# Performance work log

Measured on AMD Instinct MI355X. Metric: run time of the kernel, lower is better.

Reference implementation:

```python
import jax, jax.numpy as jnp
import numpy as np

B, NX, NY = 8, 256, 256
WIDTH, HIDDEN, M1, M2, NLAYERS = 32, 128, 16, 16, 4


def setup_inputs() -> dict:
    key = jax.random.key(0)
    ks = jax.random.split(key, 16)
    scale = 1.0 / (WIDTH * WIDTH)
    inp = {
        'bc': jax.random.normal(ks[0], (B, 3), jnp.float32),
        'x': jax.random.uniform(ks[1], (B, NX, NY), jnp.float32),
        'y': jax.random.uniform(ks[2], (B, NX, NY), jnp.float32),
        'mlp1_w': jax.random.normal(ks[3], (5, WIDTH), jnp.float32) * 0.3,
        'mlp1_b': jnp.zeros((WIDTH,), jnp.float32),
        'spec_wr': scale * jax.random.normal(ks[4], (NLAYERS, WIDTH, WIDTH, M1, M2), jnp.float32),
        'spec_wi': scale * jax.random.normal(ks[5], (NLAYERS, WIDTH, WIDTH, M1, M2), jnp.float32),
        'pw_w': jax.random.normal(ks[6], (NLAYERS, WIDTH, WIDTH), jnp.float32) * (1.0 / np.sqrt(WIDTH)),
        'pw_b': jnp.zeros((NLAYERS, WIDTH), jnp.float32),
        'dec_w1': jax.random.normal(ks[7], (3, WIDTH, WIDTH), jnp.float32) * (1.0 / np.sqrt(WIDTH)),
        'dec_b1': jnp.zeros((3, WIDTH), jnp.float32),
        'dec_w2': jax.random.normal(ks[8], (3, WIDTH, HIDDEN), jnp.float32) * (1.0 / np.sqrt(WIDTH)),
        'dec_b2': jnp.zeros((3, HIDDEN), jnp.float32),
        'dec_w3': jax.random.normal(ks[9], (3, HIDDEN, 1), jnp.float32) * (1.0 / np.sqrt(HIDDEN)),
        'dec_b3': jnp.zeros((3, 1), jnp.float32),
    }
    return inp


def _gelu(v):
    return jax.nn.gelu(v, approximate=False)  # torch F.gelu default = exact erf


def _spectral_conv(h, wr, wi):
    # h: (B, C, NX, NY)
    w = wr + 1j * wi  # (C, C, M1, M2)
    x_ft = jnp.fft.rfft2(h, norm='ortho')  # (B, C, NX, NY//2+1)
    t = jnp.einsum('bixy,ioxy->boxy', x_ft[:, :, :M1, :M2], w)
    out_ft = jnp.zeros((h.shape[0], wr.shape[1], NX, NY // 2 + 1), jnp.complex64)
    out_ft = out_ft.at[:, :, :M1, :M2].set(t)
    return jnp.fft.irfft2(out_ft, s=(NX, NY), norm='ortho')


def reference(bc, x, y, mlp1_w, mlp1_b, spec_wr, spec_wi, pw_w, pw_b,
              dec_w1, dec_b1, dec_w2, dec_b2, dec_w3, dec_b3):
    Bsz, Nx, Ny = x.shape
    bc_exp = jnp.broadcast_to(bc[:, None, None, :], (Bsz, Nx, Ny, 3))
    inp = jnp.concatenate([bc_exp, x[..., None], y[..., None]], axis=-1)  # (B,Nx,Ny,5)
    h = inp @ mlp1_w + mlp1_b  # lifting
    h = jnp.transpose(h, (0, 3, 1, 2))  # (B, W, Nx, Ny)
    for l in range(NLAYERS):
        sc = _spectral_conv(h, spec_wr[l], spec_wi[l])
        pw = jnp.einsum('bixy,oi->boxy', h, pw_w[l]) + pw_b[l][None, :, None, None]
        h = h + _gelu(sc + pw)
    hf = jnp.transpose(h, (0, 2, 3, 1))  # (B, Nx, Ny, W)
    outs = []
    for d in range(3):  # temp, pressure, velocity decoders
        z = _gelu(hf @ dec_w1[d] + dec_b1[d])
        z = _gelu(z @ dec_w2[d] + dec_b2[d])
        outs.append(z @ dec_w3[d] + dec_b3[d])  # (B,Nx,Ny,1)
    return jnp.concatenate(outs, axis=-1)
```

## Files before the change

### kernel.cpp

```cpp
#include <hip/hip_runtime.h>
#include <math.h>

#define BSZ 8
#define CW  32
#define NN  256
#define MM  16
#define NL  4
#define HID 128

typedef __attribute__((ext_vector_type(8))) short bf16x8;
typedef __attribute__((ext_vector_type(4))) short s16x4;
typedef __attribute__((ext_vector_type(4))) float f32x4;
typedef __attribute__((ext_vector_type(4))) unsigned int u32x4;

static __device__ __forceinline__ float gelu_f(float v) {
    float av = fabsf(v);
    float u  = av * 0.70710678118654752f;
    float P  = fmaf(fmaf(fmaf(fmaf(0.078108f, u, 0.000972f), u, 0.230389f),
                         u, 0.278393f), u, 1.0f);
    float r  = __builtin_amdgcn_rcpf(P);
    float r2 = r * r;
    float r4 = r2 * r2;
    return fmaf(-0.5f * av, r4, fmaxf(v, 0.0f));
}

static __device__ __forceinline__ unsigned pack_hl(float v) {
    unsigned b  = __float_as_uint(v);
    unsigned hi = b >> 16;
    float hif   = __uint_as_float(hi << 16);
    float lo    = v - hif;
    unsigned lou = __float_as_uint(lo) >> 16;
    return (hi << 16) | lou;
}

static __device__ __forceinline__ short bf16_rne(float v) {
    unsigned u = __float_as_uint(v);
    u += 0x7fffu + ((u >> 16) & 1u);
    return (short)(u >> 16);
}

#define TWO_PI_OVER_N (6.28318530717958647692f / 256.0f)

__global__ void k_prep(const float* __restrict__ w1, const float* __restrict__ w2,
                       const float* __restrict__ pww,
                       short* __restrict__ wb1h, short* __restrict__ wb1l,
                       short* __restrict__ wb2h, short* __restrict__ wb2l,
                       short* __restrict__ wpwh, short* __restrict__ wpwl,
                       short* __restrict__ wifh, short* __restrict__ wifl,
                       short* __restrict__ wfyh, short* __restrict__ wfyl) {
    int t0 = blockIdx.x * 256 + threadIdx.x;
    for (int idx = t0; idx < 3 * 2 * 16 * 32; idx += 8192) {
        int k = idx & 31, n16 = (idx >> 5) & 15, nb = (idx >> 9) & 1, d = idx >> 10;
        unsigned p = pack_hl(w1[d * 1024 + k * 32 + nb * 16 + n16]);
        wb1h[idx] = (short)(p >> 16);
        wb1l[idx] = (short)(p & 0xffffu);
    }
    for (int idx = t0; idx < 3 * 8 * 16 * 32; idx += 8192) {
        int k = idx & 31, n16 = (idx >> 5) & 15, blk = (idx >> 9) & 7, d = idx >> 12;
        unsigned p = pack_hl(w2[d * 4096 + k * 128 + blk * 16 + n16]);
        wb2h[idx] = (short)(p >> 16);
        wb2l[idx] = (short)(p & 0xffffu);
    }
    for (int idx = t0; idx < NL * 1024; idx += 8192) {
        unsigned p = pack_hl(pww[idx]);
        wpwh[idx] = (short)(p >> 16);
        wpwl[idx] = (short)(p & 0xffffu);
    }
    for (int idx = t0; idx < 16 * 64 * 8; idx += 8192) {
        int j = idx & 7, l = (idx >> 3) & 63, ntg = idx >> 9;
        int k = ((l >> 4) << 3) + j, y = (ntg << 4) + (l & 15);
        int ky = k >> 1, p = k & 1;
        float v;
        if (k == 0)      v = 1.0f / 256.0f;
        else if (k == 1) v = 0.0f;
        else {
            float ang = TWO_PI_OVER_N * (float)((ky * y) & 255);
            v = p ? (-2.0f / 256.0f) * sinf(ang) : (2.0f / 256.0f) * cosf(ang);
        }
        unsigned pb = pack_hl(v);
        wifh[idx] = (short)(pb >> 16);
        wifl[idx] = (short)(pb & 0xffffu);
    }
    for (int idx = t0; idx < 16 * 64 * 8; idx += 8192) {
        int j = idx & 7, l = (idx >> 3) & 63, f = idx >> 9;
        int nt = f & 1, kstep = f >> 1;
        int y  = (kstep >> 1) * 64 + (kstep & 1) * 32 + ((l >> 4) << 3) + j;
        int kc = nt * 16 + (l & 15);
        int ky = kc >> 1, p = kc & 1;
        float ang = TWO_PI_OVER_N * (float)((ky * y) & 255);
        float v = p ? -sinf(ang) : cosf(ang);
        unsigned pb = pack_hl(v);
        wfyh[idx] = (short)(pb >> 16);
        wfyl[idx] = (short)(pb & 0xffffu);
    }
}

static __device__ __forceinline__ void dft_y_mfma(
        const short* __restrict__ hlsh, const short* __restrict__ hlsl,
        float* __restrict__ red,
        const short* __restrict__ wfyh, const short* __restrict__ wfyl,
        float* __restrict__ gy, int b, int x, int wv, int lk, int l15, int tid) {
    f32x4 acc2[2][2];
#pragma unroll
    for (int mt = 0; mt < 2; ++mt)
#pragma unroll
        for (int nt = 0; nt < 2; ++nt) acc2[mt][nt] = (f32x4){0.f, 0.f, 0.f, 0.f};
#pragma unroll
    for (int kk = 0; kk < 2; ++kk) {
        bf16x8 ahh[2], all2[2];
#pragma unroll
        for (int mt = 0; mt < 2; ++mt) {
            int c  = mt * 16 + l15;
            int yl = (kk * 32 + lk * 8) ^ ((c & 7) << 3);
            ahh[mt]  = *(const bf16x8*)&hlsh[c * 64 + yl];
            all2[mt] = *(const bf16x8*)&hlsl[c * 64 + yl];
        }
#pragma unroll
        for (int nt = 0; nt < 2; ++nt) {
            int fb = (((wv * 2 + kk) * 2 + nt) * 64 + (tid & 63)) * 8;
            bf16x8 bh = *(const bf16x8*)&wfyh[fb];
            bf16x8 bl = *(const bf16x8*)&wfyl[fb];
#pragma unroll
            for (int mt = 0; mt < 2; ++mt) {
                f32x4 a = acc2[mt][nt];
                a = __builtin_amdgcn_mfma_f32_16x16x32_bf16(all2[mt], bh, a, 0, 0, 0);
                a = __builtin_amdgcn_mfma_f32_16x16x32_bf16(ahh[mt],  bl, a, 0, 0, 0);
                a = __builtin_amdgcn_mfma_f32_16x16x32_bf16(ahh[mt],  bh, a, 0, 0, 0);
                acc2[mt][nt] = a;
            }
        }
    }
#pragma unroll
    for (int mt = 0; mt < 2; ++mt)
#pragma unroll
        for (int nt = 0; nt < 2; ++nt)
#pragma unroll
            for (int r = 0; r < 4; ++r)
                red[(wv * 32 + mt * 16 + lk * 4 + r) * 33 + nt * 16 + l15] =
                    acc2[mt][nt][r];
    __syncthreads();
#pragma unroll
    for (int e = 0; e < 4; ++e) {
        int idx = e * 256 + tid;
        int c = idx >> 5, kc = idx & 31;
        float v = red[(c) * 33 + kc] + red[(32 + c) * 33 + kc]
                + red[(64 + c) * 33 + kc] + red[(96 + c) * 33 + kc];
        gy[((size_t)(b * 32 + c)) * 8192 + x * 32 + kc] = v;
    }
}

__global__ void __launch_bounds__(256) k_lift_fy(
        const float* __restrict__ bc, const float* __restrict__ xg,
        const float* __restrict__ yg, const float* __restrict__ w,
        const float* __restrict__ bias, float* __restrict__ h,
        const short* __restrict__ wfyh, const short* __restrict__ wfyl,
        float* __restrict__ gy) {
    __shared__ short hlsh[4][2048];
    __shared__ short hlsl[4][2048];
    __shared__ float red[4224];
    int tid = threadIdx.x;
    int wv = tid >> 6, lk = (tid >> 4) & 3, l15 = tid & 15;
    int bx = blockIdx.x, b = bx >> 8, x = bx & 255;
    int y = tid;
    float i0 = bc[b * 3 + 0], i1 = bc[b * 3 + 1], i2 = bc[b * 3 + 2];
    float i3 = xg[b * 65536 + x * 256 + y];
    float i4 = yg[b * 65536 + x * 256 + y];
    size_t hb = (((size_t)b * 32) << 16) + x * 256 + y;
#pragma unroll
    for (int c = 0; c < 32; ++c) {
        float v = i0 * w[c] + i1 * w[CW + c] + i2 * w[2 * CW + c]
                + i3 * w[3 * CW + c] + i4 * w[4 * CW + c] + bias[c];
        h[hb + ((size_t)c << 16)] = v;
        unsigned pb = pack_hl(v);
        int sl = (y & 63) ^ ((c & 7) << 3);
        hlsh[wv][c * 64 + sl] = (short)(pb >> 16);
        hlsl[wv][c * 64 + sl] = (short)(pb & 0xffffu);
    }
    dft_y_mfma(&hlsh[wv][0], &hlsl[wv][0], red, wfyh, wfyl, gy, b, x, wv, lk, l15, tid);
}

__global__ void __launch_bounds__(1024) k_fwd_x(const float* __restrict__ gy,
                                                float* __restrict__ Xf) {
    __shared__ float g[8192];
    __shared__ float part[4][256][2];
    __shared__ float ct[256], st[256];
    int tid = threadIdx.x;
    if (tid < 256) {
        float ang = (float)tid * TWO_PI_OVER_N;
        ct[tid] = cosf(ang);
        st[tid] = sinf(ang);
    }
    size_t base = (size_t)blockIdx.x * 8192;
#pragma unroll
    for (int j = 0; j < 8; ++j) g[j * 1024 + tid] = gy[base + j * 1024 + tid];
    __syncthreads();

    int t = tid & 255, xq = tid >> 8;
    int kx = t >> 4, ky = t & 15;
    float ar = 0.f, ai = 0.f;
    int x0 = xq * 64;
    int idx = (kx * x0) & 255;
#pragma unroll 4
    for (int x = x0; x < x0 + 64; ++x) {
        float c = ct[idx], s = st[idx];
        float gr = g[x * 32 + ky * 2], gi = g[x * 32 + ky * 2 + 1];
        ar += gr * c + gi * s;
        ai += gi * c - gr * s;
        idx = (idx + kx) & 255;
    }
    part[xq][t][0] = ar;
    part[xq][t][1] = ai;
    __syncthreads();
    if (tid < 256) {
        float a0 = part[0][tid][0] + part[1][tid][0] + part[2][tid][0] + part[3][tid][0];
        float a1 = part[0][tid][1] + part[1][tid][1] + part[2][tid][1] + part[3][tid][1];
        Xf[((size_t)blockIdx.x * 256 + tid) * 2 + 0] = a0 * (1.0f / 256.0f);
        Xf[((size_t)blockIdx.x * 256 + tid) * 2 + 1] = a1 * (1.0f / 256.0f);
    }
}

__global__ void __launch_bounds__(1024) k_spec(const float* __restrict__ Xf,
                                               const float* __restrict__ wr,
                                               const float* __restrict__ wi,
                                               float* __restrict__ gi) {
    __shared__ float tl[512];
    __shared__ float pp[4][256][2];
    __shared__ float ct[256], st[256];
    int tid = threadIdx.x;
    if (tid < 256) {
        float ang = (float)tid * TWO_PI_OVER_N;
        ct[tid] = cosf(ang);
        st[tid] = sinf(ang);
    }
    int b = blockIdx.x >> 5, o = blockIdx.x & 31;
    int t = tid & 255, ig = tid >> 8;

    float tr = 0.f, ti = 0.f;
    const float2* xp = (const float2*)Xf + (size_t)b * 8192 + t;
    const float* wrp = wr + (size_t)o * 256 + t;
    const float* wip = wi + (size_t)o * 256 + t;
#pragma unroll
    for (int i = ig * 8; i < ig * 8 + 8; ++i) {
        float2 xv = xp[i * 256];
        float wrv = wrp[(size_t)i * 8192];
        float wiv = wip[(size_t)i * 8192];
        tr += xv.x * wrv - xv.y * wiv;
        ti += xv.x * wiv + xv.y * wrv;
    }
    pp[ig][t][0] = tr;
    pp[ig][t][1] = ti;
    __syncthreads();
    if (tid < 256) {
        tl[tid * 2 + 0] = pp[0][tid][0] + pp[1][tid][0] + pp[2][tid][0] + pp[3][tid][0];
        tl[tid * 2 + 1] = pp[0][tid][1] + pp[1][tid][1] + pp[2][tid][1] + pp[3][tid][1];
    }
    __syncthreads();

    int x = t, kg = ig;
    float gre[4], gim[4];
#pragma unroll
    for (int k = 0; k < 4; ++k) { gre[k] = 0.f; gim[k] = 0.f; }
#pragma unroll 4
    for (int kx = 0; kx < 16; ++kx) {
        int idx = (kx * x) & 255;
        float c = ct[idx], s = st[idx];
#pragma unroll
        for (int k = 0; k < 4; ++k) {
            int ky = kg * 4 + k;
            float t2r = tl[(kx * 16 + ky) * 2 + 0];
            float t2i = tl[(kx * 16 + ky) * 2 + 1];
            gre[k] += t2r * c - t2i * s;
            gim[k] += t2i * c + t2r * s;
        }
    }
    size_t ob = (((size_t)b * 256 + x) * 32 + o) * 32;
#pragma unroll
    for (int k = 0; k < 4; ++k) {
        gi[ob + (kg * 4 + k) * 2 + 0] = gre[k];
        gi[ob + (kg * 4 + k) * 2 + 1] = gim[k];
    }
}

__global__ void __launch_bounds__(256) k_update(float* __restrict__ h,
        const float* __restrict__ gi,
        const short* __restrict__ wpwh, const short* __restrict__ wpwl,
        const float* __restrict__ pwb,
        const short* __restrict__ wifh, const short* __restrict__ wifl,
        const short* __restrict__ wfyh, const short* __restrict__ wfyl,
        float* __restrict__ gy, int do_fy) {
    __shared__ short hlsh[4][2048];
    __shared__ short hlsl[4][2048];
    __shared__ float red[4224];
    int tid = threadIdx.x;
    int wv = tid >> 6, l = tid & 63;
    int l15 = l & 15, lk = l >> 4;
    int bx = blockIdx.x, b = bx >> 8, x = bx & 255;
    float* hx = h + (((size_t)b * 32) << 16) + x * 256;

    bf16x8 gth[2], gtl[2], wh[2], wl[2];
    const float* gp = gi + (size_t)bx * 1024;
#pragma unroll
    for (int mt = 0; mt < 2; ++mt) {
        const float* ap = gp + (mt * 16 + l15) * 32 + lk * 8;
        float4 a0 = *(const float4*)ap;
        float4 a1 = *(const float4*)(ap + 4);
        float av[8] = {a0.x, a0.y, a0.z, a0.w, a1.x, a1.y, a1.z, a1.w};
#pragma unroll
        for (int j = 0; j < 8; ++j) {
            unsigned pb = pack_hl(av[j]);
            gth[mt][j] = (short)(pb >> 16);
            gtl[mt][j] = (short)(pb & 0xffffu);
        }
        int wbase = (mt * 16 + l15) * 32 + lk * 8;
        wh[mt] = *(const bf16x8*)(wpwh + wbase);
        wl[mt] = *(const bf16x8*)(wpwl + wbase);
    }

    f32x4 acc[2][4];
#pragma unroll
    for (int nt = 0; nt < 4; ++nt) {
        int y = wv * 64 + nt * 16 + l15;
        int ntg = wv * 4 + nt;
        int qb = ntg * 512 + l * 8;
        bf16x8 wih = *(const bf16x8*)(wifh + qb);
        bf16x8 wil = *(const bf16x8*)(wifl + qb);
        bf16x8 hbh, hbl;
#pragma unroll
        for (int j = 0; j < 8; ++j) {
            float v = hx[((size_t)(lk * 8 + j) << 16) + y];
            unsigned pb = pack_hl(v);
            hbh[j] = (short)(pb >> 16);
            hbl[j] = (short)(pb & 0xffffu);
        }
#pragma unroll
        for (int mt = 0; mt < 2; ++mt) {
            f32x4 a = {0.f, 0.f, 0.f, 0.f};
            a = __builtin_amdgcn_mfma_f32_16x16x32_bf16(gtl[mt], wih, a, 0, 0, 0);
            a = __builtin_amdgcn_mfma_f32_16x16x32_bf16(gth[mt], wil, a, 0, 0, 0);
            a = __builtin_amdgcn_mfma_f32_16x16x32_bf16(gth[mt], wih, a, 0, 0, 0);
            a = __builtin_amdgcn_mfma_f32_16x16x32_bf16(wl[mt],  hbh, a, 0, 0, 0);
            a = __builtin_amdgcn_mfma_f32_16x16x32_bf16(wh[mt],  hbl, a, 0, 0, 0);
            a = __builtin_amdgcn_mfma_f32_16x16x32_bf16(wh[mt],  hbh, a, 0, 0, 0);
            acc[mt][nt] = a;
        }
    }

    float hold[2][4][4];
#pragma unroll
    for (int mt = 0; mt < 2; ++mt)
#pragma unroll
        for (int nt = 0; nt < 4; ++nt) {
            int y = wv * 64 + nt * 16 + l15;
#pragma unroll
            for (int r = 0; r < 4; ++r)
                hold[mt][nt][r] = hx[((size_t)(mt * 16 + lk * 4 + r) << 16) + y];
        }
#pragma unroll
    for (int mt = 0; mt < 2; ++mt)
#pragma unroll
        for (int nt = 0; nt < 4; ++nt) {
            int y = wv * 64 + nt * 16 + l15;
#pragma unroll
            for (int r = 0; r < 4; ++r) {
                int o = mt * 16 + lk * 4 + r;
                float u = acc[mt][nt][r] + pwb[o];
                float hn = hold[mt][nt][r] + gelu_f(u);
                hx[((size_t)o << 16) + y] = hn;
                if (do_fy) {
                    unsigned pb = pack_hl(hn);
                    int sl = (nt * 16 + l15) ^ ((o & 7) << 3);
                    hlsh[wv][o * 64 + sl] = (short)(pb >> 16);
                    hlsl[wv][o * 64 + sl] = (short)(pb & 0xffffu);
                }
            }
        }
    if (do_fy)
        dft_y_mfma(&hlsh[wv][0], &hlsl[wv][0], red, wfyh, wfyl, gy,
                   b, x, wv, lk, l15, tid);
}

__global__ void __launch_bounds__(256) k_decode(const float* __restrict__ h,
        const short* __restrict__ wb1h, const short* __restrict__ wb1l,
        const float* __restrict__ b1,
        const short* __restrict__ wb2h, const short* __restrict__ wb2l,
        const float* __restrict__ b2,
        const float* __restrict__ w3, const float* __restrict__ b3,
        float* __restrict__ out) {
    __shared__ short z1s[4][64][32];
    int tid = threadIdx.x;
    int wv = tid >> 6, l = tid & 63;
    int l15 = l & 15, lk = l >> 4;
    int b = blockIdx.x >> 8;
    int pos0 = (blockIdx.x & 255) * 256;

    bf16x8 ah[4], al[4];
    const float* hb = h + (((size_t)b * 32) << 16) + pos0;
#pragma unroll
    for (int mt = 0; mt < 4; ++mt) {
        int p = wv * 64 + mt * 16 + l15;
#pragma unroll
        for (int j = 0; j < 8; ++j) {
            float v = hb[((size_t)(lk * 8 + j) << 16) + p];
            unsigned pb = pack_hl(v);
            ah[mt][j] = (short)(pb >> 16);
            al[mt][j] = (short)(pb & 0xffffu);
        }
    }

    size_t gbase = (size_t)blockIdx.x * 256 + wv * 64;
    for (int d = 0; d < 3; ++d) {
        bf16x8 w1h[2], w1l[2];
        float bias1[2];
#pragma unroll
        for (int nb = 0; nb < 2; ++nb) {
            int base = ((d * 2 + nb) * 16 + l15) * 32 + lk * 8;
            w1h[nb] = *(const bf16x8*)(wb1h + base);
            w1l[nb] = *(const bf16x8*)(wb1l + base);
            bias1[nb] = b1[d * 32 + nb * 16 + l15];
        }
#pragma unroll
        for (int mt = 0; mt < 4; ++mt) {
#pragma unroll
            for (int nb = 0; nb < 2; ++nb) {
                f32x4 acc = {0.f, 0.f, 0.f, 0.f};
                acc = __builtin_amdgcn_mfma_f32_16x16x32_bf16(al[mt], w1h[nb], acc, 0, 0, 0);
                acc = __builtin_amdgcn_mfma_f32_16x16x32_bf16(ah[mt], w1l[nb], acc, 0, 0, 0);
                acc = __builtin_amdgcn_mfma_f32_16x16x32_bf16(ah[mt], w1h[nb], acc, 0, 0, 0);
                int c = nb * 16 + l15;
#pragma unroll
                for (int r = 0; r < 4; ++r) {
                    float z = gelu_f(acc[r] + bias1[nb]);
                    int rw = mt * 16 + lk * 4 + r;
                    z1s[wv][rw][(((c >> 2) ^ (rw & 7)) << 2) | (c & 3)] = bf16_rne(z);
                }
            }
        }
        bf16x8 zah[4];
#pragma unroll
        for (int mt = 0; mt < 4; ++mt) {
            int rwr = mt * 16 + l15;
            int sl0 = (2 * lk) ^ (rwr & 7);
            int sl1 = (2 * lk + 1) ^ (rwr & 7);
            s16x4 q0 = *(const s16x4*)&z1s[wv][rwr][sl0 << 2];
            s16x4 q1 = *(const s16x4*)&z1s[wv][rwr][sl1 << 2];
#pragma unroll
            for (int j = 0; j < 4; ++j) {
                zah[mt][j]     = q0[j];
                zah[mt][4 + j] = q1[j];
            }
        }
        float p3[4][4];
#pragma unroll
        for (int mt = 0; mt < 4; ++mt)
#pragma unroll
            for (int r = 0; r < 4; ++r) p3[mt][r] = 0.f;
#pragma unroll 2
        for (int blk = 0; blk < 8; ++blk) {
            int base = ((d * 8 + blk) * 16 + l15) * 32 + lk * 8;
            bf16x8 bh  = *(const bf16x8*)(wb2h + base);
            bf16x8 bl2 = *(const bf16x8*)(wb2l + base);
            float bias2 = b2[d * 128 + blk * 16 + l15];
            float w3v   = w3[d * 128 + blk * 16 + l15];
#pragma unroll
            for (int mt = 0; mt < 4; ++mt) {
                f32x4 acc = {0.f, 0.f, 0.f, 0.f};
                acc = __builtin_amdgcn_mfma_f32_16x16x32_bf16(zah[mt], bl2, acc, 0, 0, 0);
                acc = __builtin_amdgcn_mfma_f32_16x16x32_bf16(zah[mt], bh, acc, 0, 0, 0);
#pragma unroll
                for (int r = 0; r < 4; ++r)
                    p3[mt][r] = fmaf(gelu_f(acc[r] + bias2), w3v, p3[mt][r]);
            }
        }
        float b3d = b3[d];
#pragma unroll
        for (int mt = 0; mt < 4; ++mt) {
#pragma unroll
            for (int r = 0; r < 4; ++r) {
                float v = p3[mt][r];
                v += __shfl_xor(v, 1, 64);
                v += __shfl_xor(v, 2, 64);
                v += __shfl_xor(v, 4, 64);
                v += __shfl_xor(v, 8, 64);
                if (l15 == r)
                    out[(gbase + mt * 16 + lk * 4 + r) * 3 + d] = v + b3d;
            }
        }
    }
}

extern "C" void kernel_launch(void* const* d_in, const int* in_sizes, int n_in,
                              void* d_out, int out_size, void* d_ws, size_t ws_size,
                              hipStream_t stream) {
    const float* bc      = (const float*)d_in[0];
    const float* xg      = (const float*)d_in[1];
    const float* yg      = (const float*)d_in[2];
    const float* mlp1_w  = (const float*)d_in[3];
    const float* mlp1_b  = (const float*)d_in[4];
    const float* spec_wr = (const float*)d_in[5];
    const float* spec_wi = (const float*)d_in[6];
    const float* pw_w    = (const float*)d_in[7];
    const float* pw_b    = (const float*)d_in[8];
    const float* dec_w1  = (const float*)d_in[9];
    const float* dec_b1  = (const float*)d_in[10];
    const float* dec_w2  = (const float*)d_in[11];
    const float* dec_b2  = (const float*)d_in[12];
    const float* dec_w3  = (const float*)d_in[13];
    const float* dec_b3  = (const float*)d_in[14];
    float* out = (float*)d_out;

    float* h    = (float*)d_ws;
    float* gi   = h + 16777216;
    float* gy   = gi + 2097152;
    float* Xf   = gy + 2097152;
    short* wb1h = (short*)(Xf + 131072);
    short* wb1l = wb1h + 3072;
    short* wb2h = wb1l + 3072;
    short* wb2l = wb2h + 12288;
    short* wpwh = wb2l + 12288;
    short* wpwl = wpwh + 4096;
    short* wifh = wpwl + 4096;
    short* wifl = wifh + 8192;
    short* wfyh = wifl + 8192;
    short* wfyl = wfyh + 8192;
    (void)ws_size; (void)n_in; (void)in_sizes; (void)out_size;

    k_prep<<<32, 256, 0, stream>>>(dec_w1, dec_w2, pw_w,
                                   wb1h, wb1l, wb2h, wb2l,
                                   wpwh, wpwl, wifh, wifl, wfyh, wfyl);
    k_lift_fy<<<2048, 256, 0, stream>>>(bc, xg, yg, mlp1_w, mlp1_b, h,
                                        wfyh, wfyl, gy);
    for (int l = 0; l < NL; ++l) {
        k_fwd_x<<<256, 1024, 0, stream>>>(gy, Xf);
        k_spec<<<256, 1024, 0, stream>>>(Xf, spec_wr + (size_t)l * 262144,
                                         spec_wi + (size_t)l * 262144, gi);
        k_update<<<2048, 256, 0, stream>>>(h, gi, wpwh + l * 1024, wpwl + l * 1024,
                                           pw_b + l * 32, wifh, wifl,
                                           wfyh, wfyl, gy, (l < NL - 1) ? 1 : 0);
    }
    k_decode<<<2048, 256, 0, stream>>>(h, wb1h, wb1l, dec_b1, wb2h, wb2l, dec_b2,
                                       dec_w3, dec_b3, out);
}
```

Baseline: 338.6 us.

## Fuse decoder into final update kernel and fold GELU polynomial constant

The final layer's update kernel now runs the three decoder MLPs directly from the bf16 hi/lo tiles already staged in shared memory. This removes the separate decode launch, the last write of h to global memory and the re-read of h. The reduction buffer is reused as the decoder's z1 scratch, which raises register and LDS pressure in the update kernel. The GELU erf approximation is also rewritten with the 1/sqrt(2) scale folded into the polynomial coefficients, saving one multiply per call.

Measured after the change: 356.1 us. 5.2% more time.

```diff
diff --git a/kernel.cpp b/kernel.cpp
--- a/kernel.cpp
+++ b/kernel.cpp
@@ -15,9 +15,8 @@
 
 static __device__ __forceinline__ float gelu_f(float v) {
     float av = fabsf(v);
-    float u  = av * 0.70710678118654752f;
-    float P  = fmaf(fmaf(fmaf(fmaf(0.078108f, u, 0.000972f), u, 0.230389f),
-                         u, 0.278393f), u, 1.0f);
+    float P  = fmaf(fmaf(fmaf(fmaf(0.01952700f, av, 0.00034365f), av, 0.11519450f),
+                         av, 0.19685434f), av, 1.0f);
     float r  = __builtin_amdgcn_rcpf(P);
     float r2 = r * r;
     float r4 = r2 * r2;
@@ -287,10 +286,17 @@
         const float* __restrict__ pwb,
         const short* __restrict__ wifh, const short* __restrict__ wifl,
         const short* __restrict__ wfyh, const short* __restrict__ wfyl,
-        float* __restrict__ gy, int do_fy) {
+        float* __restrict__ gy, int do_fy, int do_dec,
+        const short* __restrict__ wb1h, const short* __restrict__ wb1l,
+        const float* __restrict__ b1,
+        const short* __restrict__ wb2h, const short* __restrict__ wb2l,
+        const float* __restrict__ b2,
+        const float* __restrict__ w3, const float* __restrict__ b3,
+        float* __restrict__ out) {
     __shared__ short hlsh[4][2048];
     __shared__ short hlsl[4][2048];
-    __shared__ float red[4224];
+    __shared__ char  ubuf[16896];
+    float* red = (float*)ubuf;
     int tid = threadIdx.x;
     int wv = tid >> 6, l = tid & 63;
     int l15 = l & 15, lk = l >> 4;
@@ -365,124 +371,107 @@
                 int o = mt * 16 + lk * 4 + r;
                 float u = acc[mt][nt][r] + pwb[o];
                 float hn = hold[mt][nt][r] + gelu_f(u);
-                hx[((size_t)o << 16) + y] = hn;
-                if (do_fy) {
-                    unsigned pb = pack_hl(hn);
-                    int sl = (nt * 16 + l15) ^ ((o & 7) << 3);
-                    hlsh[wv][o * 64 + sl] = (short)(pb >> 16);
-                    hlsl[wv][o * 64 + sl] = (short)(pb & 0xffffu);
-                }
+                if (!do_dec) hx[((size_t)o << 16) + y] = hn;
+                unsigned pb = pack_hl(hn);
+                int sl = (nt * 16 + l15) ^ ((o & 7) << 3);
+                hlsh[wv][o * 64 + sl] = (short)(pb >> 16);
+                hlsl[wv][o * 64 + sl] = (short)(pb & 0xffffu);
             }
         }
     if (do_fy)
         dft_y_mfma(&hlsh[wv][0], &hlsl[wv][0], red, wfyh, wfyl, gy,
                    b, x, wv, lk, l15, tid);
-}
-
-__global__ void __launch_bounds__(256) k_decode(const float* __restrict__ h,
-        const short* __restrict__ wb1h, const short* __restrict__ wb1l,
-        const float* __restrict__ b1,
-        const short* __restrict__ wb2h, const short* __restrict__ wb2l,
-        const float* __restrict__ b2,
-        const float* __restrict__ w3, const float* __restrict__ b3,
-        float* __restrict__ out) {
-    __shared__ short z1s[4][64][32];
-    int tid = threadIdx.x;
-    int wv = tid >> 6, l = tid & 63;
-    int l15 = l & 15, lk = l >> 4;
-    int b = blockIdx.x >> 8;
-    int pos0 = (blockIdx.x & 255) * 256;
-
-    bf16x8 ah[4], al[4];
-    const float* hb = h + (((size_t)b * 32) << 16) + pos0;
-#pragma unroll
-    for (int mt = 0; mt < 4; ++mt) {
-        int p = wv * 64 + mt * 16 + l15;
-#pragma unroll
-        for (int j = 0; j < 8; ++j) {
-            float v = hb[((size_t)(lk * 8 + j) << 16) + p];
-            unsigned pb = pack_hl(v);
-            ah[mt][j] = (short)(pb >> 16);
-            al[mt][j] = (short)(pb & 0xffffu);
-        }
-    }
-
-    size_t gbase = (size_t)blockIdx.x * 256 + wv * 64;
-    for (int d = 0; d < 3; ++d) {
-        bf16x8 w1h[2], w1l[2];
-        float bias1[2];
-#pragma unroll
-        for (int nb = 0; nb < 2; ++nb) {
-            int base = ((d * 2 + nb) * 16 + l15) * 32 + lk * 8;
-            w1h[nb] = *(const bf16x8*)(wb1h + base);
-            w1l[nb] = *(const bf16x8*)(wb1l + base);
-            bias1[nb] = b1[d * 32 + nb * 16 + l15];
-        }
+
+    if (do_dec) {
+        short* z1b = (short*)ubuf + wv * 64 * 32;
+        bf16x8 ah[4], al[4];
 #pragma unroll
         for (int mt = 0; mt < 4; ++mt) {
 #pragma unroll
+            for (int j = 0; j < 8; ++j) {
+                int c = lk * 8 + j;
+                int sl = (mt * 16 + l15) ^ ((c & 7) << 3);
+                ah[mt][j] = hlsh[wv][c * 64 + sl];
+                al[mt][j] = hlsl[wv][c * 64 + sl];
+            }
+        }
+        size_t gbase = (size_t)bx * 256 + wv * 64;
+        for (int d = 0; d < 3; ++d) {
+            bf16x8 w1h[2], w1l[2];
+            float bias1[2];
+#pragma unroll
             for (int nb = 0; nb < 2; ++nb) {
-                f32x4 acc = {0.f, 0.f, 0.f, 0.f};
-                acc = __builtin_amdgcn_mfma_f32_16x16x32_bf16(al[mt], w1h[nb], acc, 0, 0, 0);
-                acc = __builtin_amdgcn_mfma_f32_16x16x32_bf16(ah[mt], w1l[nb], acc, 0, 0, 0);
-                acc = __builtin_amdgcn_mfma_f32_16x16x32_bf16(ah[mt], w1h[nb], acc, 0, 0, 0);
-                int c = nb * 16 + l15;
+                int base = ((d * 2 + nb) * 16 + l15) * 32 + lk * 8;
+                w1h[nb] = *(const bf16x8*)(wb1h + base);
+                w1l[nb] = *(const bf16x8*)(wb1l + base);
+                bias1[nb] = b1[d * 32 + nb * 16 + l15];
+            }
+#pragma unroll
+            for (int mt = 0; mt < 4; ++mt) {
+#pragma unroll
+                for (int nb = 0; nb < 2; ++nb) {
+                    f32x4 acc2 = {0.f, 0.f, 0.f, 0.f};
+                    acc2 = __builtin_amdgcn_mfma_f32_16x16x32_bf16(al[mt], w1h[nb], acc2, 0, 0, 0);
+                    acc2 = __builtin_amdgcn_mfma_f32_16x16x32_bf16(ah[mt], w1l[nb], acc2, 0, 0, 0);
+                    acc2 = __builtin_amdgcn_mfma_f32_16x16x32_bf16(ah[mt], w1h[nb], acc2, 0, 0, 0);
+                    int c = nb * 16 + l15;
+#pragma unroll
+                    for (int r = 0; r < 4; ++r) {
+                        float z = gelu_f(acc2[r] + bias1[nb]);
+                        int rw = mt * 16 + lk * 4 + r;
+                        z1b[rw * 32 + ((((c >> 2) ^ (rw & 7)) << 2) | (c & 3))] = bf16_rne(z);
+                    }
+                }
+            }
+            bf16x8 zah[4];
+#pragma unroll
+            for (int mt = 0; mt < 4; ++mt) {
+                int rwr = mt * 16 + l15;
+                int sl0 = (2 * lk) ^ (rwr & 7);
+                int sl1 = (2 * lk + 1) ^ (rwr & 7);
+                s16x4 q0 = *(const s16x4*)&z1b[rwr * 32 + (sl0 << 2)];
+                s16x4 q1 = *(const s16x4*)&z1b[rwr * 32 + (sl1 << 2)];
+#pragma unroll
+                for (int j = 0; j < 4; ++j) {
+                    zah[mt][j]     = q0[j];
+                    zah[mt][4 + j] = q1[j];
+                }
+            }
+            float p3[4][4];
+#pragma unroll
+            for (int mt = 0; mt < 4; ++mt)
+#pragma unroll
+                for (int r = 0; r < 4; ++r) p3[mt][r] = 0.f;
+#pragma unroll 2
+            for (int blk = 0; blk < 8; ++blk) {
+                int base = ((d * 8 + blk) * 16 + l15) * 32 + lk * 8;
+                bf16x8 bh  = *(const bf16x8*)(wb2h + base);
+                bf16x8 bl2 = *(const bf16x8*)(wb2l + base);
+                float bias2 = b2[d * 128 + blk * 16 + l15];
+                float w3v   = w3[d * 128 + blk * 16 + l15];
+#pragma unroll
+                for (int mt = 0; mt < 4; ++mt) {
+                    f32x4 acc2 = {0.f, 0.f, 0.f, 0.f};
+                    acc2 = __builtin_amdgcn_mfma_f32_16x16x32_bf16(zah[mt], bl2, acc2, 0, 0, 0);
+                    acc2 = __builtin_amdgcn_mfma_f32_16x16x32_bf16(zah[mt], bh, acc2, 0, 0, 0);
+#pragma unroll
+                    for (int r = 0; r < 4; ++r)
+                        p3[mt][r] = fmaf(gelu_f(acc2[r] + bias2), w3v, p3[mt][r]);
+                }
+            }
+            float b3d = b3[d];
+#pragma unroll
+            for (int mt = 0; mt < 4; ++mt) {
 #pragma unroll
                 for (int r = 0; r < 4; ++r) {
-                    float z = gelu_f(acc[r] + bias1[nb]);
-                    int rw = mt * 16 + lk * 4 + r;
-                    z1s[wv][rw][(((c >> 2) ^ (rw & 7)) << 2) | (c & 3)] = bf16_rne(z);
+                    float v = p3[mt][r];
+                    v += __shfl_xor(v, 1, 64);
+                    v += __shfl_xor(v, 2, 64);
+                    v += __shfl_xor(v, 4, 64);
+                    v += __shfl_xor(v, 8, 64);
+                    if (l15 == r)
+                        out[(gbase + mt * 16 + lk * 4 + r) * 3 + d] = v + b3d;
                 }
-            }
-        }
-        bf16x8 zah[4];
-#pragma unroll
-        for (int mt = 0; mt < 4; ++mt) {
-            int rwr = mt * 16 + l15;
-            int sl0 = (2 * lk) ^ (rwr & 7);
-            int sl1 = (2 * lk + 1) ^ (rwr & 7);
-            s16x4 q0 = *(const s16x4*)&z1s[wv][rwr][sl0 << 2];
-            s16x4 q1 = *(const s16x4*)&z1s[wv][rwr][sl1 << 2];
-#pragma unroll
-            for (int j = 0; j < 4; ++j) {
-                zah[mt][j]     = q0[j];
-                zah[mt][4 + j] = q1[j];
-            }
-        }
-        float p3[4][4];
-#pragma unroll
-        for (int mt = 0; mt < 4; ++mt)
-#pragma unroll
-            for (int r = 0; r < 4; ++r) p3[mt][r] = 0.f;
-#pragma unroll 2
-        for (int blk = 0; blk < 8; ++blk) {
-            int base = ((d * 8 + blk) * 16 + l15) * 32 + lk * 8;
-            bf16x8 bh  = *(const bf16x8*)(wb2h + base);
-            bf16x8 bl2 = *(const bf16x8*)(wb2l + base);
-            float bias2 = b2[d * 128 + blk * 16 + l15];
-            float w3v   = w3[d * 128 + blk * 16 + l15];
-#pragma unroll
-            for (int mt = 0; mt < 4; ++mt) {
-                f32x4 acc = {0.f, 0.f, 0.f, 0.f};
-                acc = __builtin_amdgcn_mfma_f32_16x16x32_bf16(zah[mt], bl2, acc, 0, 0, 0);
-                acc = __builtin_amdgcn_mfma_f32_16x16x32_bf16(zah[mt], bh, acc, 0, 0, 0);
-#pragma unroll
-                for (int r = 0; r < 4; ++r)
-                    p3[mt][r] = fmaf(gelu_f(acc[r] + bias2), w3v, p3[mt][r]);
-            }
-        }
-        float b3d = b3[d];
-#pragma unroll
-        for (int mt = 0; mt < 4; ++mt) {
-#pragma unroll
-            for (int r = 0; r < 4; ++r) {
-                float v = p3[mt][r];
-                v += __shfl_xor(v, 1, 64);
-                v += __shfl_xor(v, 2, 64);
-                v += __shfl_xor(v, 4, 64);
-                v += __shfl_xor(v, 8, 64);
-                if (l15 == r)
-                    out[(gbase + mt * 16 + lk * 4 + r) * 3 + d] = v + b3d;
             }
         }
     }
@@ -533,10 +522,11 @@
         k_fwd_x<<<256, 1024, 0, stream>>>(gy, Xf);
         k_spec<<<256, 1024, 0, stream>>>(Xf, spec_wr + (size_t)l * 262144,
                                          spec_wi + (size_t)l * 262144, gi);
+        int last = (l == NL - 1);
         k_update<<<2048, 256, 0, stream>>>(h, gi, wpwh + l * 1024, wpwl + l * 1024,
                                            pw_b + l * 32, wifh, wifl,
-                                           wfyh, wfyl, gy, (l < NL - 1) ? 1 : 0);
-    }
-    k_decode<<<2048, 256, 0, stream>>>(h, wb1h, wb1l, dec_b1, wb2h, wb2l, dec_b2,
-                                       dec_w3, dec_b3, out);
-}
+                                           wfyh, wfyl, gy, last ? 0 : 1, last ? 1 : 0,
+                                           wb1h, wb1l, dec_b1, wb2h, wb2l, dec_b2,
+                                           dec_w3, dec_b3, out);
+    }
+}
```
